# Performance work log

Hardware: AMD Instinct MI355X
Metric: run time of the kernel (lower is better)

The kernel has to match this reference:

```python
import jax, jax.numpy as jnp
import numpy as np
from jax import lax

TOPK = 80
RADIUS_GAIN = 14.0
RADIUS_MIN = 1.5
RADIUS_MAX = 18.0


def _norm01(x, eps=1e-6):
    b = x.shape[0]
    flat = x.reshape(b, -1)
    mn = flat.min(axis=1).reshape(b, 1, 1, 1)
    mx = flat.max(axis=1).reshape(b, 1, 1, 1)
    return (x - mn) / (mx - mn + eps)


def _avg_pool9(x):
    # kernel 9, stride 1, pad 4, count_include_pad=True (torch default)
    s = lax.reduce_window(x, 0.0, lax.add, (1, 1, 9, 9), (1, 1, 1, 1),
                          [(0, 0), (0, 0), (4, 4), (4, 4)])
    return s / 81.0


def _max_pool5(x):
    return lax.reduce_window(x, -jnp.inf, lax.max, (1, 1, 5, 5), (1, 1, 1, 1),
                             [(0, 0), (0, 0), (2, 2), (2, 2)])


def setup_inputs() -> dict:
    key = jax.random.key(0)
    k1, k2 = jax.random.split(key)
    B, H, W = 8, 256, 256
    voxel_score_map = jax.random.uniform(k1, (B, 1, H, W), dtype=jnp.float32)
    depth = jax.random.uniform(k2, (B, 1, H, W), dtype=jnp.float32)
    return {"voxel_score_map": voxel_score_map, "depth": depth}


def reference(voxel_score_map, depth):
    dtype = voxel_score_map.dtype
    b, _, h, w = voxel_score_map.shape

    # _compact_connected_prior
    occ = (voxel_score_map > 0.2).astype(dtype)
    local_occ = _avg_pool9(occ)
    local_mass = _avg_pool9(voxel_score_map)
    compact = _norm01(local_occ * local_mass)
    score_map = voxel_score_map * compact

    # _gaussian_map: 5x5 max-pool NMS -> per-image top-k peaks
    pooled = _max_pool5(score_map)
    maxima = score_map * (score_map == pooled).astype(dtype)
    flat = maxima[:, 0].reshape(b, h * w)          # [b, h*w]
    vals, inds = lax.top_k(flat, TOPK)             # [b, k]
    vals = jnp.where(vals > 0, vals, jnp.zeros_like(vals))  # masked peaks splat 0
    ys = (inds // w).astype(dtype)
    xs = (inds % w).astype(dtype)

    z = jnp.take_along_axis(depth[:, 0].reshape(b, h * w), inds, axis=1)
    z = jnp.maximum(z, 0.001)
    radius = jnp.clip(RADIUS_GAIN / z, RADIUS_MIN, RADIUS_MAX)  # [b, k]
    sigma2 = (0.6 * radius) ** 2                                 # [b, k]

    yy = jnp.arange(h, dtype=dtype)
    xx = jnp.arange(w, dtype=dtype)
    dx = xx[None, None, None, :] - xs[:, :, None, None]   # [b, k, 1, w]
    dy = yy[None, None, :, None] - ys[:, :, None, None]   # [b, k, h, 1]
    d2 = dx ** 2 + dy ** 2                                 # [b, k, h, w]
    maps = vals[:, :, None, None] * jnp.exp(-d2 / (2.0 * sigma2[:, :, None, None] + 1e-6))
    gauss = maps.max(axis=1)[:, None]                      # [b, 1, h, w]
    return _norm01(gauss)
```

## Files before the change

### kernel.cpp

```cpp
#include <hip/hip_runtime.h>
#include <float.h>
#include <math.h>

#define BB 8
#define HH 256
#define WW 256
#define NPIX 65536
#define TOT (BB*NPIX)
#define KTOP 80
#define NTIL 64
#define TCAP 128
#define CAP 8192
#define SELBINS 4096
#define BNDCAP 4096
#define NBLK (BB*NTIL)
typedef unsigned long long ull;

__global__ void k_box9(const float* __restrict__ vsm, float* __restrict__ prod,
                       float* __restrict__ pmn,
                       unsigned* __restrict__ histg, unsigned* __restrict__ bcnt) {
    int blk = blockIdx.x;
    int b = blk >> 6, t = blk & 63;
    int ty0 = (t >> 3) << 5, tx0 = (t & 7) << 5;
    int tid = threadIdx.x;

    if (tid < 64) histg[b * SELBINS + t * 64 + tid] = 0u;
    if (blk < BB && tid == 0) bcnt[blk] = 0u;

    __shared__ float val[40][40];
    __shared__ float rs_o[40][32];
    __shared__ float rs_m[40][32];
    for (int i = tid; i < 1600; i += 256) {
        int ly = i / 40, lx = i - ly * 40;
        int gy = ty0 - 4 + ly, gx = tx0 - 4 + lx;
        float v = 0.f;
        if (gy >= 0 && gy < HH && gx >= 0 && gx < WW) v = vsm[(b * HH + gy) * WW + gx];
        val[ly][lx] = v;
    }
    __syncthreads();
    for (int i = tid; i < 1280; i += 256) {
        int ly = i >> 5, lx = i & 31;
        float so = 0.f, sm = 0.f;
        #pragma unroll
        for (int d = 0; d < 9; ++d) { float v = val[ly][lx + d]; so += (v > 0.2f) ? 1.f : 0.f; sm += v; }
        rs_o[ly][lx] = so; rs_m[ly][lx] = sm;
    }
    __syncthreads();
    int ox = tid & 31, oy0 = (tid >> 5) << 2;
    float tmn = FLT_MAX;
    #pragma unroll
    for (int j = 0; j < 4; ++j) {
        int oy = oy0 + j;
        float so = 0.f, sm = 0.f;
        #pragma unroll
        for (int d = 0; d < 9; ++d) { so += rs_o[oy + d][ox]; sm += rs_m[oy + d][ox]; }
        float p = (so * (1.f / 81.f)) * (sm * (1.f / 81.f));
        prod[(b * HH + ty0 + oy) * WW + tx0 + ox] = p;
        tmn = fminf(tmn, p);
    }
    #pragma unroll
    for (int o = 32; o > 0; o >>= 1) tmn = fminf(tmn, __shfl_xor(tmn, o, 64));
    __shared__ float wmn[4];
    if ((tid & 63) == 0) wmn[tid >> 6] = tmn;
    __syncthreads();
    if (tid == 0) pmn[blk] = fminf(fminf(wmn[0], wmn[1]), fminf(wmn[2], wmn[3]));
}

__global__ void k_nms(const float* __restrict__ vsm, const float* __restrict__ prod,
                      const float* __restrict__ pmn,
                      unsigned* __restrict__ bcnt, float* __restrict__ candV,
                      int* __restrict__ candI, unsigned* __restrict__ histg) {
    int blk = blockIdx.x;
    int b = blk >> 6, t = blk & 63;
    int ty0 = (t >> 3) << 5, tx0 = (t & 7) << 5;
    int tid = threadIdx.x;
    __shared__ float sredn;
    if (tid < 64) {
        float mn = pmn[b * NTIL + tid];
        #pragma unroll
        for (int o = 32; o > 0; o >>= 1) mn = fminf(mn, __shfl_xor(mn, o, 64));
        if (tid == 0) sredn = mn;
    }
    __syncthreads();
    float mnp = sredn;
    __shared__ float sc[36][36];
    __shared__ float hm[36][32];
    for (int i = tid; i < 1296; i += 256) {
        int ly = i / 36, lx = i - ly * 36;
        int gy = ty0 - 2 + ly, gx = tx0 - 2 + lx;
        float s = -FLT_MAX;
        if (gy >= 0 && gy < HH && gx >= 0 && gx < WW) {
            int idx = (b * HH + gy) * WW + gx;
            s = vsm[idx] * (prod[idx] - mnp);
        }
        sc[ly][lx] = s;
    }
    __syncthreads();
    for (int i = tid; i < 1152; i += 256) {
        int ly = i >> 5, lx = i & 31;
        float m = sc[ly][lx];
        #pragma unroll
        for (int d = 1; d < 5; ++d) m = fmaxf(m, sc[ly][lx + d]);
        hm[ly][lx] = m;
    }
    __syncthreads();
    __shared__ unsigned scnt;
    __shared__ unsigned sbase;
    __shared__ float bv[TCAP];
    __shared__ int bi[TCAP];
    if (tid == 0) scnt = 0;
    __syncthreads();
    int ox = tid & 31, oy0 = (tid >> 5) << 2;
    #pragma unroll
    for (int j = 0; j < 4; ++j) {
        int oy = oy0 + j;
        float m = hm[oy][ox];
        #pragma unroll
        for (int d = 1; d < 5; ++d) m = fmaxf(m, hm[oy + d][ox]);
        float s = sc[oy + 2][ox + 2];
        if (s == m && s > 0.f) {
            unsigned p = atomicAdd(&scnt, 1u);
            if (p < TCAP) { bv[p] = s; bi[p] = (ty0 + oy) * WW + tx0 + ox; }
        }
    }
    __syncthreads();
    unsigned cnt = min(scnt, (unsigned)TCAP);
    if (tid == 0) sbase = cnt ? atomicAdd(&bcnt[b], cnt) : 0u;
    __syncthreads();
    unsigned base = sbase;
    for (unsigned i = tid; i < cnt; i += 256) {
        unsigned pos = base + i;
        if (pos < CAP) {
            float v = bv[i];
            candV[b * CAP + pos] = v;
            candI[b * CAP + pos] = bi[i];
            atomicAdd(&histg[b * SELBINS + (__float_as_uint(v) >> 19)], 1u);
        }
    }
}

__global__ void __launch_bounds__(1024)
k_topk(const float* __restrict__ depth, const unsigned* __restrict__ bcnt,
       const float* __restrict__ candV, const int* __restrict__ candI,
       const unsigned* __restrict__ histg, float4* __restrict__ pk,
       float* __restrict__ vmaxg) {
    int b = blockIdx.x;
    int tid = threadIdx.x;
    __shared__ unsigned sc[1024];
    __shared__ ull bnd[BNDCAP];
    __shared__ ull acc[KTOP];
    __shared__ int sBin;
    __shared__ unsigned nAccS, nBndS, svm;

    const unsigned* hg = histg + b * SELBINS;
    int j0 = tid * 4;
    unsigned h0 = hg[j0], h1 = hg[j0 + 1], h2 = hg[j0 + 2], h3 = hg[j0 + 3];
    unsigned part = h0 + h1 + h2 + h3;
    sc[tid] = part;
    if (tid == 0) { sBin = 0; nAccS = 0; nBndS = 0; svm = 0; }
    __syncthreads();
    for (int off = 1; off < 1024; off <<= 1) {
        unsigned v = (tid + off < 1024) ? sc[tid + off] : 0u;
        __syncthreads();
        sc[tid] += v;
        __syncthreads();
    }
    unsigned excl = sc[tid] - part;
    unsigned suf3 = excl + h3, suf2 = suf3 + h2, suf1 = suf2 + h1, suf0 = suf1 + h0;
    if (suf0 >= KTOP && suf0 - h0 < KTOP) sBin = j0;
    if (suf1 >= KTOP && suf1 - h1 < KTOP) sBin = j0 + 1;
    if (suf2 >= KTOP && suf2 - h2 < KTOP) sBin = j0 + 2;
    if (suf3 >= KTOP && suf3 - h3 < KTOP) sBin = j0 + 3;
    __syncthreads();
    int B = sBin;

    int nC = min((int)bcnt[b], CAP);
    for (int i = tid; i < nC; i += 1024) {
        float v = candV[b * CAP + i];
        unsigned bits = __float_as_uint(v);
        int bin = (int)(bits >> 19);
        if (bin >= B) {
            ull key = ((ull)bits << 32) | (ull)(0xFFFFFFFFu - (unsigned)candI[b * CAP + i]);
            if (bin > B) {
                unsigned p = atomicAdd(&nAccS, 1u);
                if (p < KTOP) acc[p] = key;
            } else {
                unsigned q = atomicAdd(&nBndS, 1u);
                if (q < BNDCAP) bnd[q] = key;
            }
        }
    }
    __syncthreads();
    unsigned nAcc = min(nAccS, (unsigned)KTOP);
    unsigned nBnd = min(nBndS, (unsigned)BNDCAP);
    unsigned quota = (KTOP > nAcc) ? (KTOP - nAcc) : 0u;
    if (quota > nBnd) quota = nBnd;

    for (int i = tid; i < (int)nBnd; i += 1024) {
        ull mykey = bnd[i];
        unsigned rank = 0;
        for (unsigned j = 0; j < nBnd; ++j) rank += (bnd[j] > mykey) ? 1u : 0u;
        if (rank < quota) acc[nAcc + rank] = mykey;
    }
    __syncthreads();

    unsigned nTot = nAcc + quota;
    if (tid < KTOP) {
        ull key = ((unsigned)tid < nTot) ? acc[tid] : 0ull;
        float plog = -INFINITY, fx = 0.f, fy = 0.f, c = 0.f;
        if (key) {
            unsigned bits = (unsigned)(key >> 32);
            atomicMax(&svm, bits);
            int idx = (int)(0xFFFFFFFFu - (unsigned)(key & 0xFFFFFFFFu));
            float val = __uint_as_float(bits);
            plog = log2f(val);
            fx = (float)(idx & 255);
            fy = (float)(idx >> 8);
            float z = fmaxf(depth[b * NPIX + idx], 0.001f);
            float r = fminf(fmaxf(14.f / z, 1.5f), 18.f);
            float s2 = 0.36f * r * r;
            c = 1.44269504f / (2.f * s2 + 1e-6f);
        }
        pk[b * KTOP + tid] = make_float4(plog, fx, fy, c);
    }
    __syncthreads();
    if (tid == 0) vmaxg[b] = __uint_as_float(svm);
}

__global__ void __launch_bounds__(256)
k_splat(const float4* __restrict__ pk, const float* __restrict__ vmaxg,
        float* __restrict__ out) {
    int blk = blockIdx.x;
    int b = blk >> 6;
    int y0 = (blk & 63) << 2;
    int x = threadIdx.x;
    __shared__ float4 lp[KTOP];
    __shared__ float4 lpf[KTOP];
    __shared__ unsigned fcnt;
    if (x == 0) fcnt = 0;
    if (x < KTOP) lp[x] = pk[b * KTOP + x];
    __syncthreads();

    float vmax = vmaxg[b];
    float thr = log2f(vmax + 1e-30f) - 11.f;

    if (x < KTOP) {
        float4 q = lp[x];
        float dymin = 0.f;
        if (q.z < (float)y0) dymin = (float)y0 - q.z;
        else if (q.z > (float)(y0 + 3)) dymin = q.z - (float)(y0 + 3);
        if (q.x - dymin * dymin * q.w >= thr) {
            unsigned p = atomicAdd(&fcnt, 1u);
            lpf[p] = q;
        }
    }
    __syncthreads();
    int m = (int)fcnt;

    float fx = (float)x, fy = (float)y0;
    float g0 = -INFINITY, g1 = -INFINITY, g2 = -INFINITY, g3 = -INFINITY;
    #pragma unroll 4
    for (int k = 0; k < m; ++k) {
        float4 q = lpf[k];
        float dx = fx - q.y;
        float dx2 = dx * dx;
        float dy = fy - q.z;
        float d2;
        d2 = fmaf(dy, dy, dx2);          g0 = fmaxf(g0, fmaf(-d2, q.w, q.x));
        float dyb = dy + 1.f;
        d2 = fmaf(dyb, dyb, dx2);        g1 = fmaxf(g1, fmaf(-d2, q.w, q.x));
        float dyc = dy + 2.f;
        d2 = fmaf(dyc, dyc, dx2);        g2 = fmaxf(g2, fmaf(-d2, q.w, q.x));
        float dyd = dy + 3.f;
        d2 = fmaf(dyd, dyd, dx2);        g3 = fmaxf(g3, fmaf(-d2, q.w, q.x));
    }
    float inv = 1.f / (vmax + 1e-6f);
    int base = (b * HH + y0) * WW + x;
    out[base]          = exp2f(g0) * inv;
    out[base + WW]     = exp2f(g1) * inv;
    out[base + 2 * WW] = exp2f(g2) * inv;
    out[base + 3 * WW] = exp2f(g3) * inv;
}

extern "C" void kernel_launch(void* const* d_in, const int* in_sizes, int n_in,
                              void* d_out, int out_size, void* d_ws, size_t ws_size,
                              hipStream_t stream) {
    const float* vsm   = (const float*)d_in[0];
    const float* depth = (const float*)d_in[1];
    float* out = (float*)d_out;

    float4* pk   = (float4*)d_ws;
    float* vmaxg = (float*)(pk + BB * KTOP);
    float* prod  = vmaxg + BB;
    float* pmn   = prod + TOT;
    unsigned* bcnt  = (unsigned*)(pmn + NBLK);
    unsigned* histg = bcnt + BB;
    float* candV = (float*)(histg + BB * SELBINS);
    int*   candI = (int*)(candV + BB * CAP);

    k_box9 <<<NBLK, 256, 0, stream>>>(vsm, prod, pmn, histg, bcnt);
    k_nms  <<<NBLK, 256, 0, stream>>>(vsm, prod, pmn, bcnt, candV, candI, histg);
    k_topk <<<BB, 1024, 0, stream>>>(depth, bcnt, candV, candI, histg, pk, vmaxg);
    k_splat<<<NBLK, 256, 0, stream>>>(pk, vmaxg, out);
}
```

Before: 38.80 us.

## Fuse top-k selection into splat kernel, recomputing selection per block

Merges the per-image top-k kernel and the splat kernel into one launch. Each of the 512 splat blocks now redoes the histogram threshold search (a wave-shuffle suffix scan instead of a 1024-thread shared scan), filters the candidates and ranks the boundary bin before splatting its own rows. This removes one kernel launch and the workspace round trip for peaks and vmax. The cost is repeated selection work in every block, and the boundary buffer is cut to 1024 entries, which could drop keys if the boundary bin is crowded.

```diff
diff --git a/kernel.cpp b/kernel.cpp
--- a/kernel.cpp
+++ b/kernel.cpp
@@ -12,7 +12,7 @@
 #define TCAP 128
 #define CAP 8192
 #define SELBINS 4096
-#define BNDCAP 4096
+#define BNDCAP 1024
 #define NBLK (BB*NTIL)
 typedef unsigned long long ull;
 
@@ -139,48 +139,67 @@
     }
 }
 
-__global__ void __launch_bounds__(1024)
-k_topk(const float* __restrict__ depth, const unsigned* __restrict__ bcnt,
-       const float* __restrict__ candV, const int* __restrict__ candI,
-       const unsigned* __restrict__ histg, float4* __restrict__ pk,
-       float* __restrict__ vmaxg) {
-    int b = blockIdx.x;
+__global__ void __launch_bounds__(256)
+k_tsplat(const float* __restrict__ depth, const unsigned* __restrict__ bcnt,
+         const float* __restrict__ candV, const int* __restrict__ candI,
+         const unsigned* __restrict__ histg, float* __restrict__ out) {
+    int blk = blockIdx.x;
+    int b = blk >> 6;
+    int y0 = (blk & 63) << 2;
     int tid = threadIdx.x;
-    __shared__ unsigned sc[1024];
+    int lane = tid & 63;
+    int wid = tid >> 6;
+
+    __shared__ ull acc[KTOP];
     __shared__ ull bnd[BNDCAP];
-    __shared__ ull acc[KTOP];
-    __shared__ int sBin;
-    __shared__ unsigned nAccS, nBndS, svm;
-
-    const unsigned* hg = histg + b * SELBINS;
-    int j0 = tid * 4;
-    unsigned h0 = hg[j0], h1 = hg[j0 + 1], h2 = hg[j0 + 2], h3 = hg[j0 + 3];
-    unsigned part = h0 + h1 + h2 + h3;
-    sc[tid] = part;
-    if (tid == 0) { sBin = 0; nAccS = 0; nBndS = 0; svm = 0; }
-    __syncthreads();
-    for (int off = 1; off < 1024; off <<= 1) {
-        unsigned v = (tid + off < 1024) ? sc[tid + off] : 0u;
+    __shared__ float4 lpf[KTOP];
+    __shared__ unsigned wtot[4];
+    __shared__ int sB;
+    __shared__ unsigned sAbove, nAccS, nBndS, svm, fcnt;
+
+    if (tid == 0) { sB = 0; sAbove = 0; nAccS = 0; nBndS = 0; svm = 0; fcnt = 0; }
+    if (tid < KTOP) acc[tid] = 0ull;
+    __syncthreads();
+
+    {
+        const unsigned* hg = histg + b * SELBINS;
+        int j0 = tid * 16;
+        unsigned h[16]; unsigned part = 0;
+        #pragma unroll
+        for (int j = 0; j < 16; j += 4) {
+            uint4 q = *reinterpret_cast<const uint4*>(hg + j0 + j);
+            h[j] = q.x; h[j+1] = q.y; h[j+2] = q.z; h[j+3] = q.w;
+            part += q.x + q.y + q.z + q.w;
+        }
+        unsigned suf = part;
+        #pragma unroll
+        for (int off = 1; off < 64; off <<= 1) {
+            unsigned v = __shfl_down(suf, off, 64);
+            if (lane + off < 64) suf += v;
+        }
+        if (lane == 0) wtot[wid] = suf;
         __syncthreads();
-        sc[tid] += v;
+        unsigned above_waves = 0;
+        #pragma unroll
+        for (int w = 0; w < 4; ++w) if (w > wid) above_waves += wtot[w];
+        unsigned run = above_waves + (suf - part);
+        for (int j = 15; j >= 0; --j) {
+            unsigned hj = h[j];
+            run += hj;
+            if (run >= KTOP && run - hj < KTOP) { sB = j0 + j; sAbove = run - hj; }
+        }
         __syncthreads();
     }
-    unsigned excl = sc[tid] - part;
-    unsigned suf3 = excl + h3, suf2 = suf3 + h2, suf1 = suf2 + h1, suf0 = suf1 + h0;
-    if (suf0 >= KTOP && suf0 - h0 < KTOP) sBin = j0;
-    if (suf1 >= KTOP && suf1 - h1 < KTOP) sBin = j0 + 1;
-    if (suf2 >= KTOP && suf2 - h2 < KTOP) sBin = j0 + 2;
-    if (suf3 >= KTOP && suf3 - h3 < KTOP) sBin = j0 + 3;
-    __syncthreads();
-    int B = sBin;
+    int B = sB;
 
     int nC = min((int)bcnt[b], CAP);
-    for (int i = tid; i < nC; i += 1024) {
+    for (int i = tid; i < nC; i += 256) {
         float v = candV[b * CAP + i];
         unsigned bits = __float_as_uint(v);
         int bin = (int)(bits >> 19);
         if (bin >= B) {
             ull key = ((ull)bits << 32) | (ull)(0xFFFFFFFFu - (unsigned)candI[b * CAP + i]);
+            atomicMax(&svm, bits);
             if (bin > B) {
                 unsigned p = atomicAdd(&nAccS, 1u);
                 if (p < KTOP) acc[p] = key;
@@ -196,7 +215,7 @@
     unsigned quota = (KTOP > nAcc) ? (KTOP - nAcc) : 0u;
     if (quota > nBnd) quota = nBnd;
 
-    for (int i = tid; i < (int)nBnd; i += 1024) {
+    for (int i = tid; i < (int)nBnd; i += 256) {
         ull mykey = bnd[i];
         unsigned rank = 0;
         for (unsigned j = 0; j < nBnd; ++j) rank += (bnd[j] > mykey) ? 1u : 0u;
@@ -204,78 +223,52 @@
     }
     __syncthreads();
 
+    float vmax = __uint_as_float(svm);
+    float thr = log2f(vmax + 1e-30f) - 11.f;
     unsigned nTot = nAcc + quota;
-    if (tid < KTOP) {
-        ull key = ((unsigned)tid < nTot) ? acc[tid] : 0ull;
-        float plog = -INFINITY, fx = 0.f, fy = 0.f, c = 0.f;
+    if (tid < (int)nTot) {
+        ull key = acc[tid];
         if (key) {
             unsigned bits = (unsigned)(key >> 32);
-            atomicMax(&svm, bits);
             int idx = (int)(0xFFFFFFFFu - (unsigned)(key & 0xFFFFFFFFu));
             float val = __uint_as_float(bits);
-            plog = log2f(val);
-            fx = (float)(idx & 255);
-            fy = (float)(idx >> 8);
+            float plog = log2f(val);
+            float fy = (float)(idx >> 8);
             float z = fmaxf(depth[b * NPIX + idx], 0.001f);
             float r = fminf(fmaxf(14.f / z, 1.5f), 18.f);
             float s2 = 0.36f * r * r;
-            c = 1.44269504f / (2.f * s2 + 1e-6f);
-        }
-        pk[b * KTOP + tid] = make_float4(plog, fx, fy, c);
-    }
-    __syncthreads();
-    if (tid == 0) vmaxg[b] = __uint_as_float(svm);
-}
-
-__global__ void __launch_bounds__(256)
-k_splat(const float4* __restrict__ pk, const float* __restrict__ vmaxg,
-        float* __restrict__ out) {
-    int blk = blockIdx.x;
-    int b = blk >> 6;
-    int y0 = (blk & 63) << 2;
-    int x = threadIdx.x;
-    __shared__ float4 lp[KTOP];
-    __shared__ float4 lpf[KTOP];
-    __shared__ unsigned fcnt;
-    if (x == 0) fcnt = 0;
-    if (x < KTOP) lp[x] = pk[b * KTOP + x];
-    __syncthreads();
-
-    float vmax = vmaxg[b];
-    float thr = log2f(vmax + 1e-30f) - 11.f;
-
-    if (x < KTOP) {
-        float4 q = lp[x];
-        float dymin = 0.f;
-        if (q.z < (float)y0) dymin = (float)y0 - q.z;
-        else if (q.z > (float)(y0 + 3)) dymin = q.z - (float)(y0 + 3);
-        if (q.x - dymin * dymin * q.w >= thr) {
-            unsigned p = atomicAdd(&fcnt, 1u);
-            lpf[p] = q;
+            float c = 1.44269504f / (2.f * s2 + 1e-6f);
+            float dymin = 0.f;
+            if (fy < (float)y0) dymin = (float)y0 - fy;
+            else if (fy > (float)(y0 + 3)) dymin = fy - (float)(y0 + 3);
+            if (plog - dymin * dymin * c >= thr) {
+                unsigned p = atomicAdd(&fcnt, 1u);
+                lpf[p] = make_float4(plog, (float)(idx & 255), fy, c);
+            }
         }
     }
     __syncthreads();
     int m = (int)fcnt;
 
-    float fx = (float)x, fy = (float)y0;
+    float fx = (float)tid, fyv = (float)y0;
     float g0 = -INFINITY, g1 = -INFINITY, g2 = -INFINITY, g3 = -INFINITY;
     #pragma unroll 4
     for (int k = 0; k < m; ++k) {
         float4 q = lpf[k];
         float dx = fx - q.y;
         float dx2 = dx * dx;
-        float dy = fy - q.z;
+        float dy = fyv - q.z;
         float d2;
-        d2 = fmaf(dy, dy, dx2);          g0 = fmaxf(g0, fmaf(-d2, q.w, q.x));
+        d2 = fmaf(dy, dy, dx2);              g0 = fmaxf(g0, fmaf(-d2, q.w, q.x));
         float dyb = dy + 1.f;
-        d2 = fmaf(dyb, dyb, dx2);        g1 = fmaxf(g1, fmaf(-d2, q.w, q.x));
+        d2 = fmaf(dyb, dyb, dx2);            g1 = fmaxf(g1, fmaf(-d2, q.w, q.x));
         float dyc = dy + 2.f;
-        d2 = fmaf(dyc, dyc, dx2);        g2 = fmaxf(g2, fmaf(-d2, q.w, q.x));
+        d2 = fmaf(dyc, dyc, dx2);            g2 = fmaxf(g2, fmaf(-d2, q.w, q.x));
         float dyd = dy + 3.f;
-        d2 = fmaf(dyd, dyd, dx2);        g3 = fmaxf(g3, fmaf(-d2, q.w, q.x));
+        d2 = fmaf(dyd, dyd, dx2);            g3 = fmaxf(g3, fmaf(-d2, q.w, q.x));
     }
     float inv = 1.f / (vmax + 1e-6f);
-    int base = (b * HH + y0) * WW + x;
+    int base = (b * HH + y0) * WW + tid;
     out[base]          = exp2f(g0) * inv;
     out[base + WW]     = exp2f(g1) * inv;
     out[base + 2 * WW] = exp2f(g2) * inv;
@@ -289,17 +282,14 @@
     const float* depth = (const float*)d_in[1];
     float* out = (float*)d_out;
 
-    float4* pk   = (float4*)d_ws;
-    float* vmaxg = (float*)(pk + BB * KTOP);
-    float* prod  = vmaxg + BB;
+    float* prod  = (float*)d_ws;
     float* pmn   = prod + TOT;
     unsigned* bcnt  = (unsigned*)(pmn + NBLK);
     unsigned* histg = bcnt + BB;
     float* candV = (float*)(histg + BB * SELBINS);
     int*   candI = (int*)(candV + BB * CAP);
 
-    k_box9 <<<NBLK, 256, 0, stream>>>(vsm, prod, pmn, histg, bcnt);
-    k_nms  <<<NBLK, 256, 0, stream>>>(vsm, prod, pmn, bcnt, candV, candI, histg);
-    k_topk <<<BB, 1024, 0, stream>>>(depth, bcnt, candV, candI, histg, pk, vmaxg);
-    k_splat<<<NBLK, 256, 0, stream>>>(pk, vmaxg, out);
-}
+    k_box9  <<<NBLK, 256, 0, stream>>>(vsm, prod, pmn, histg, bcnt);
+    k_nms   <<<NBLK, 256, 0, stream>>>(vsm, prod, pmn, bcnt, candV, candI, histg);
+    k_tsplat<<<NBLK, 256, 0, stream>>>(depth, bcnt, candV, candI, histg, out);
+}
```

Result: faster. 36.28 us (-6.5%).
